# Optimization experiments

Hardware: AMD Instinct MI355X
Metric: run time of the kernel (lower is better)

The kernel has to match this reference:

```python
import jax, jax.numpy as jnp
import numpy as np

BIT = 8
QMAX = 2 ** (BIT - 1) - 1          # 127
QMIN = -(2 ** (BIT - 1))           # -128
BOUNDARY_RANGE = 0.005
EPS = 1e-5


def _quant_act_int8(x):
    # StatsQ per-tensor activation quantization: scale from (1 - boundary_range)
    # quantile of |x| (robust absmax), fake-quant with STE.
    amax = jnp.maximum(jnp.quantile(jnp.abs(x), 1.0 - BOUNDARY_RANGE), EPS)
    s = QMAX / amax
    q = jnp.clip(jnp.round(x * s), QMIN, QMAX) / s
    return x + jax.lax.stop_gradient(q - x)


def _quant_w_ternary(w):
    # BitNet-1.58-style per-tensor ternary weight quantization:
    # gamma = mean(|W|); W_q in {-1, 0, +1} * gamma; STE.
    gamma = jnp.mean(jnp.abs(w)) + EPS
    q = jnp.clip(jnp.round(w / gamma), -1.0, 1.0) * gamma
    return w + jax.lax.stop_gradient(q - w)


def _qlinear(x, w):
    # quantize activations (int8 fake-quant) and weights (ternary), then matmul
    xq = _quant_act_int8(x)
    wq = _quant_w_ternary(w)
    return jnp.einsum('btd,hd->bth', xq, wq)


def _layernorm(x, g, b):
    mu = jnp.mean(x, axis=-1, keepdims=True)
    var = jnp.mean(jnp.square(x - mu), axis=-1, keepdims=True)
    return (x - mu) * jax.lax.rsqrt(var + 1e-5) * g + b


def setup_inputs() -> dict:
    key = jax.random.key(0)
    k_x, k_w1, k_w2 = jax.random.split(key, 3)
    B, T, D, H = 64, 256, 1024, 4096
    x = jax.random.normal(k_x, (B, T, D), dtype=jnp.float32)
    ln_g = jnp.ones((D,), dtype=jnp.float32)
    ln_b = jnp.zeros((D,), dtype=jnp.float32)
    w1 = jax.random.normal(k_w1, (H, D), dtype=jnp.float32) * (1.0 / np.sqrt(D))
    w2 = jax.random.normal(k_w2, (D, H), dtype=jnp.float32) * (1.0 / np.sqrt(H))
    return {'x': x, 'ln_g': ln_g, 'ln_b': ln_b, 'w1': w1, 'w2': w2}


def reference(x, ln_g, ln_b, w1, w2):
    h = _layernorm(x, ln_g, ln_b)          # [B,T,D]
    h = _qlinear(h, w1)                    # [B,T,H]
    h = jax.nn.gelu(h, approximate=False)  # torch nn.GELU default = exact erf
    out = _qlinear(h, w2)                  # [B,T,D]
    return out
```

## Files before the change

kernel.cpp:

```cpp
#include <hip/hip_runtime.h>
#include <hip/hip_fp16.h>
#include <math.h>


#define M_ROWS 16384
#define D_DIM  1024
#define H_DIM  4096

typedef int i32x4 __attribute__((ext_vector_type(4)));
typedef int i32x16 __attribute__((ext_vector_type(16)));

#define AS1 __attribute__((address_space(1)))
#define AS3 __attribute__((address_space(3)))

__device__ __forceinline__ void load_lds16(const void* g, void* l) {
  __builtin_amdgcn_global_load_lds((const AS1 void*)g, (AS3 void*)l, 16, 0, 0);
}

__device__ __forceinline__ float block_sum256(float v, float* lds) {
#pragma unroll
  for (int o = 32; o > 0; o >>= 1) v += __shfl_down(v, o, 64);
  int t = threadIdx.x;
  __syncthreads();
  if ((t & 63) == 0) lds[t >> 6] = v;
  __syncthreads();
  return lds[0] + lds[1] + lds[2] + lds[3];
}

__global__ __launch_bounds__(256) void k_layernorm(
    const float* __restrict__ x, const float* __restrict__ g,
    const float* __restrict__ b, __half* __restrict__ out) {
  __shared__ float lds[4];
  int row = blockIdx.x, t = threadIdx.x;
  float4 v = ((const float4*)(x + (size_t)row * D_DIM))[t];
  float s = v.x + v.y + v.z + v.w;
  s = block_sum256(s, lds);
  float mu = s * (1.0f / D_DIM);
  float d0 = v.x - mu, d1 = v.y - mu, d2 = v.z - mu, d3 = v.w - mu;
  float ss = d0 * d0 + d1 * d1 + d2 * d2 + d3 * d3;
  ss = block_sum256(ss, lds);
  float inv = 1.0f / sqrtf(ss * (1.0f / D_DIM) + 1e-5f);
  float4 gg = ((const float4*)g)[t];
  float4 bb = ((const float4*)b)[t];
  __half2 p0 = __floats2half2_rn(d0 * inv * gg.x + bb.x, d1 * inv * gg.y + bb.y);
  __half2 p1 = __floats2half2_rn(d2 * inv * gg.z + bb.z, d3 * inv * gg.w + bb.w);
  uint2 st;
  st.x = *(unsigned*)&p0;
  st.y = *(unsigned*)&p1;
  ((uint2*)(out + (size_t)row * D_DIM))[t] = st;
}

__global__ __launch_bounds__(256) void k_absmean2(const float4* __restrict__ w1,
                                                  const float4* __restrict__ w2,
                                                  size_t n4, double* __restrict__ out) {
  int which = (blockIdx.x >= (gridDim.x >> 1)) ? 1 : 0;
  const float4* p = which ? w2 : w1;
  unsigned half_grid = gridDim.x >> 1;
  unsigned blk = blockIdx.x - which * half_grid;
  double s = 0.0;
  size_t stride = (size_t)half_grid * blockDim.x;
  for (size_t i = (size_t)blk * blockDim.x + threadIdx.x; i < n4; i += stride) {
    float4 v = p[i];
    s += (double)fabsf(v.x) + (double)fabsf(v.y) + (double)fabsf(v.z) + (double)fabsf(v.w);
  }
#pragma unroll
  for (int o = 32; o > 0; o >>= 1) s += __shfl_down(s, o, 64);
  __shared__ double ds[4];
  int t = threadIdx.x;
  if ((t & 63) == 0) ds[t >> 6] = s;
  __syncthreads();
  if (t == 0) atomicAdd(out + which, ds[0] + ds[1] + ds[2] + ds[3]);
}

__device__ __forceinline__ int tern1(float w, float gamma) {
  return (int)fminf(1.f, fmaxf(-1.f, rintf(w / gamma)));
}

__global__ __launch_bounds__(256) void k_wquant2(const float4* __restrict__ w1,
                                                 const float4* __restrict__ w2,
                                                 unsigned* __restrict__ q1,
                                                 unsigned* __restrict__ q2, size_t n4,
                                                 const double* __restrict__ sump,
                                                 double inv_n, float* __restrict__ gamma_out) {
  int which = (blockIdx.x >= (gridDim.x >> 1)) ? 1 : 0;
  const float4* w = which ? w2 : w1;
  unsigned* wq = which ? q2 : q1;
  unsigned half_grid = gridDim.x >> 1;
  unsigned blk = blockIdx.x - which * half_grid;
  float gamma = (float)(sump[which] * inv_n) + 1e-5f;
  if (blk == 0 && threadIdx.x == 0) gamma_out[which] = gamma;
  size_t stride = (size_t)half_grid * blockDim.x;
  for (size_t i = (size_t)blk * blockDim.x + threadIdx.x; i < n4; i += stride) {
    float4 v = w[i];
    int a = tern1(v.x, gamma), b = tern1(v.y, gamma), c = tern1(v.z, gamma), d = tern1(v.w, gamma);
    wq[i] = (unsigned)(a & 255) | ((unsigned)(b & 255) << 8) |
            ((unsigned)(c & 255) << 16) | ((unsigned)(d & 255) << 24);
  }
}

__global__ __launch_bounds__(512) void k_hist16(const uint4* __restrict__ p, size_t n8,
                                                unsigned* __restrict__ hist) {
  extern __shared__ unsigned h[];
  int t = threadIdx.x;
  for (int i = t; i < 32768; i += 512) h[i] = 0;
  __syncthreads();
  size_t stride = (size_t)gridDim.x * 512;
  for (size_t i = (size_t)blockIdx.x * 512 + t; i < n8; i += stride) {
    uint4 u = p[i];
    atomicAdd(&h[u.x & 0x7FFFu], 1u);
    atomicAdd(&h[(u.x >> 16) & 0x7FFFu], 1u);
    atomicAdd(&h[u.y & 0x7FFFu], 1u);
    atomicAdd(&h[(u.y >> 16) & 0x7FFFu], 1u);
    atomicAdd(&h[u.z & 0x7FFFu], 1u);
    atomicAdd(&h[(u.z >> 16) & 0x7FFFu], 1u);
    atomicAdd(&h[u.w & 0x7FFFu], 1u);
    atomicAdd(&h[(u.w >> 16) & 0x7FFFu], 1u);
  }
  __syncthreads();
  for (int i = t; i < 32768; i += 512) {
    unsigned c = h[i];
    if (c) atomicAdd(&hist[i], c);
  }
}

__global__ __launch_bounds__(256) void k_scanq(const unsigned* __restrict__ hist,
                                               float* __restrict__ scl,
                                               unsigned long long k, double frac) {
  __shared__ unsigned tsum[256];
  __shared__ unsigned long long pre[256];
  __shared__ unsigned vk, vk1;
  int t = threadIdx.x;
  unsigned s = 0;
  for (int j = 0; j < 128; ++j) s += hist[t * 128 + j];
  tsum[t] = s;
  __syncthreads();
  if (t == 0) {
    unsigned long long c = 0;
    for (int i = 0; i < 256; ++i) { pre[i] = c; c += tsum[i]; }
  }
  __syncthreads();
  unsigned long long base = pre[t];
  for (int j = 0; j < 128; ++j) {
    unsigned c = hist[t * 128 + j];
    if (base <= k && k < base + c) vk = t * 128 + j;
    if (base <= k + 1 && k + 1 < base + c) vk1 = t * 128 + j;
    base += c;
  }
  __syncthreads();
  if (t == 0) {
    double a = (double)__half2float(__ushort_as_half((unsigned short)vk));
    double b = (double)__half2float(__ushort_as_half((unsigned short)vk1));
    double qv = (frac >= 0.5) ? (b - (b - a) * (1.0 - frac)) : (a + (b - a) * frac);
    float amax = fmaxf((float)qv, 1e-5f);
    scl[0] = amax;
    scl[1] = 127.0f / amax;
  }
}

__device__ __forceinline__ void unpack8(uint4 u, float* f) {
  __half2 h;
  h = *(__half2*)&u.x; f[0] = __low2float(h); f[1] = __high2float(h);
  h = *(__half2*)&u.y; f[2] = __low2float(h); f[3] = __high2float(h);
  h = *(__half2*)&u.z; f[4] = __low2float(h); f[5] = __high2float(h);
  h = *(__half2*)&u.w; f[6] = __low2float(h); f[7] = __high2float(h);
}

__device__ __forceinline__ unsigned qpack4(float a, float b, float c, float d, float s) {
  int qa = (int)fminf(127.f, fmaxf(-128.f, rintf(a * s)));
  int qb = (int)fminf(127.f, fmaxf(-128.f, rintf(b * s)));
  int qc = (int)fminf(127.f, fmaxf(-128.f, rintf(c * s)));
  int qd = (int)fminf(127.f, fmaxf(-128.f, rintf(d * s)));
  return (unsigned)(qa & 255) | ((unsigned)(qb & 255) << 8) |
         ((unsigned)(qc & 255) << 16) | ((unsigned)(qd & 255) << 24);
}

__global__ __launch_bounds__(256) void k_quant16(const uint4* __restrict__ p,
                                                 uint2* __restrict__ q, size_t n8,
                                                 const float* __restrict__ scl) {
  float s = scl[1];
  size_t stride = (size_t)gridDim.x * blockDim.x;
  for (size_t i = (size_t)blockIdx.x * blockDim.x + threadIdx.x; i < n8; i += stride) {
    float f[8];
    unpack8(p[i], f);
    uint2 r;
    r.x = qpack4(f[0], f[1], f[2], f[3], s);
    r.y = qpack4(f[4], f[5], f[6], f[7], s);
    q[i] = r;
  }
}

__device__ __forceinline__ float gelu_fast(float v) {
  float a = fabsf(v) * 0.70710678118654752f;
  float t = __builtin_amdgcn_rcpf(fmaf(0.3275911f, a, 1.0f));
  float p = t * fmaf(t, fmaf(t, fmaf(t, fmaf(t, 1.061405429f, -1.453152027f),
                                     1.421413741f), -0.284496736f), 0.254829592f);
  float e = __expf(-a * a);
  float er = fmaf(-p, e, 1.0f);
  float erf_s = copysignf(er, v);
  return 0.5f * v * (1.0f + erf_s);
}

template <int K, bool GELU>
__global__ __launch_bounds__(512, 2) void k_gemm(const signed char* __restrict__ A,
                                                 const signed char* __restrict__ B,
                                                 int N, void* __restrict__ outp,
                                                 const float* __restrict__ gamma_p,
                                                 const float* __restrict__ scl) {
  constexpr int NT = K / 64;
  extern __shared__ __align__(16) char smem[];
  signed char* As = (signed char*)smem;
  signed char* Bs = (signed char*)smem + 65536;

  const int tid = threadIdx.x;
  const int lane = tid & 63;
  const int wv = tid >> 6;
  const int wr = (wv >> 2) * 128;
  const int wc = (wv & 3) * 64;

  const unsigned nwg = gridDim.x;
  const unsigned q8 = nwg >> 3;
  const unsigned bid = blockIdx.x;
  const unsigned swz = (bid & 7) * q8 + (bid >> 3);
  const unsigned nx = (unsigned)N >> 8;
  const int n0 = (int)(swz % nx) * 256;
  const int m0 = (int)(swz / nx) * 256;

  const int srow0 = tid >> 2;
  const int srow1 = srow0 + 128;
  const int scg = (tid & 3) ^ ((srow0 >> 1) & 3);
  const signed char* aG0 = A + (size_t)(m0 + srow0) * K + scg * 16;
  const signed char* aG1 = A + (size_t)(m0 + srow1) * K + scg * 16;
  const signed char* bG0 = B + (size_t)(n0 + srow0) * K + scg * 16;
  const signed char* bG1 = B + (size_t)(n0 + srow1) * K + scg * 16;
  const int sL0 = tid * 16;
  const int sL1 = sL0 + 8192;

#define STAGE_A(t_) { const int bo_ = ((t_) & 3) * 16384;            \
    load_lds16(aG0 + (size_t)(t_) * 64, As + bo_ + sL0);             \
    load_lds16(aG1 + (size_t)(t_) * 64, As + bo_ + sL1); }
#define STAGE_B(t_) { const int bo_ = ((t_) & 3) * 16384;            \
    load_lds16(bG0 + (size_t)(t_) * 64, Bs + bo_ + sL0);             \
    load_lds16(bG1 + (size_t)(t_) * 64, Bs + bo_ + sL1); }

  int a_off[4][2], b_off[2][2];
#pragma unroll
  for (int mi = 0; mi < 4; ++mi) {
    int am = wr + mi * 32 + (lane & 31);
#pragma unroll
    for (int ksl = 0; ksl < 2; ++ksl) {
      int g = ksl * 2 + (lane >> 5);
      a_off[mi][ksl] = am * 64 + ((g ^ ((am >> 1) & 3)) << 4);
    }
  }
#pragma unroll
  for (int ni = 0; ni < 2; ++ni) {
    int bn = wc + ni * 32 + (lane & 31);
#pragma unroll
    for (int ksl = 0; ksl < 2; ++ksl) {
      int g = ksl * 2 + (lane >> 5);
      b_off[ni][ksl] = bn * 64 + ((g ^ ((bn >> 1) & 3)) << 4);
    }
  }

  i32x16 acc[4][2];
#pragma unroll
  for (int mi = 0; mi < 4; ++mi)
#pragma unroll
    for (int ni = 0; ni < 2; ++ni) acc[mi][ni] = (i32x16)(0);

  STAGE_A(0); STAGE_B(0);
  STAGE_A(1); STAGE_B(1);
  STAGE_A(2); STAGE_B(2);
  asm volatile("s_waitcnt vmcnt(8)" ::: "memory");
  __builtin_amdgcn_s_barrier();

#pragma unroll 4
  for (int t = 0; t < NT; ++t) {
    const int bo = (t & 3) * 16384;
    {
      i32x4 af[4], bf[2];
#pragma unroll
      for (int mi = 0; mi < 4; ++mi) af[mi] = *(const i32x4*)(As + bo + a_off[mi][0]);
#pragma unroll
      for (int ni = 0; ni < 2; ++ni) bf[ni] = *(const i32x4*)(Bs + bo + b_off[ni][0]);
      if (t + 3 < NT) STAGE_A(t + 3);
      __builtin_amdgcn_sched_barrier(0);
      __builtin_amdgcn_s_barrier();
      __builtin_amdgcn_s_setprio(1);
#pragma unroll
      for (int mi = 0; mi < 4; ++mi)
#pragma unroll
        for (int ni = 0; ni < 2; ++ni)
          acc[mi][ni] = __builtin_amdgcn_mfma_i32_32x32x32_i8(af[mi], bf[ni], acc[mi][ni], 0, 0, 0);
      __builtin_amdgcn_s_setprio(0);
    }
    {
      i32x4 af[4], bf[2];
#pragma unroll
      for (int mi = 0; mi < 4; ++mi) af[mi] = *(const i32x4*)(As + bo + a_off[mi][1]);
#pragma unroll
      for (int ni = 0; ni < 2; ++ni) bf[ni] = *(const i32x4*)(Bs + bo + b_off[ni][1]);
      if (t + 3 < NT) STAGE_B(t + 3);
      __builtin_amdgcn_sched_barrier(0);
      __builtin_amdgcn_s_barrier();
      __builtin_amdgcn_s_setprio(1);
#pragma unroll
      for (int mi = 0; mi < 4; ++mi)
#pragma unroll
        for (int ni = 0; ni < 2; ++ni)
          acc[mi][ni] = __builtin_amdgcn_mfma_i32_32x32x32_i8(af[mi], bf[ni], acc[mi][ni], 0, 0, 0);
      __builtin_amdgcn_s_setprio(0);
    }
    if (t < NT - 3)       { asm volatile("s_waitcnt vmcnt(8)" ::: "memory"); }
    else if (t == NT - 3) { asm volatile("s_waitcnt vmcnt(4)" ::: "memory"); }
    else                  { asm volatile("s_waitcnt vmcnt(0)" ::: "memory"); }
    __builtin_amdgcn_s_barrier();
  }
#undef STAGE_A
#undef STAGE_B

  const float cs = (*gamma_p) / scl[1];
  const int col0 = n0 + wc + (lane & 31);
  const int row0 = m0 + wr + 4 * (lane >> 5);
#pragma unroll
  for (int mi = 0; mi < 4; ++mi) {
#pragma unroll
    for (int ni = 0; ni < 2; ++ni) {
      const int col = col0 + ni * 32;
#pragma unroll
      for (int reg = 0; reg < 16; ++reg) {
        const int row = row0 + mi * 32 + (reg & 3) + 8 * (reg >> 2);
        float v = cs * (float)acc[mi][ni][reg];
        size_t idx = (size_t)row * N + col;
        if (GELU) {
          ((__half*)outp)[idx] = __float2half(gelu_fast(v));
        } else {
          ((float*)outp)[idx] = v;
        }
      }
    }
  }
}

extern "C" void kernel_launch(void* const* d_in, const int* in_sizes, int n_in,
                              void* d_out, int out_size, void* d_ws, size_t ws_size,
                              hipStream_t stream) {
  const float* x = (const float*)d_in[0];
  const float* ln_g = (const float*)d_in[1];
  const float* ln_b = (const float*)d_in[2];
  const float* w1 = (const float*)d_in[3];
  const float* w2 = (const float*)d_in[4];
  float* out = (float*)d_out;

  char* ws = (char*)d_ws;
  __half* h2 = (__half*)ws;
  __half* h1 = (__half*)(ws + ((size_t)128 << 20));
  signed char* xq1 = (signed char*)(ws + ((size_t)160 << 20));
  signed char* xq2 = (signed char*)(ws + ((size_t)128 << 20));
  signed char* w1q = (signed char*)(ws + ((size_t)192 << 20));
  signed char* w2q = (signed char*)(ws + ((size_t)196 << 20));
  char* sm = ws + ((size_t)200 << 20);
  unsigned* hista = (unsigned*)sm;
  unsigned* histb = (unsigned*)(sm + (128 << 10));
  double* wsum = (double*)(sm + (256 << 10));
  float* gamma = (float*)(sm + (256 << 10) + 16);
  float* scl1 = (float*)(sm + (256 << 10) + 32);
  float* scl2 = (float*)(sm + (256 << 10) + 40);

  hipMemsetAsync(sm, 0, (256 << 10) + 64, stream);
  hipFuncSetAttribute((const void*)k_hist16, hipFuncAttributeMaxDynamicSharedMemorySize,
                      131072);
  hipFuncSetAttribute((const void*)(k_gemm<D_DIM, true>),
                      hipFuncAttributeMaxDynamicSharedMemorySize, 131072);
  hipFuncSetAttribute((const void*)(k_gemm<H_DIM, false>),
                      hipFuncAttributeMaxDynamicSharedMemorySize, 131072);

  const double qq = 1.0 - 0.005;
  const unsigned long long N1 = (unsigned long long)M_ROWS * D_DIM;
  const unsigned long long N2 = (unsigned long long)M_ROWS * H_DIM;
  double idx1 = qq * (double)(N1 - 1);
  double idx2 = qq * (double)(N2 - 1);
  unsigned long long k1 = (unsigned long long)idx1;
  unsigned long long k2 = (unsigned long long)idx2;
  double frac1 = idx1 - (double)k1;
  double frac2 = idx2 - (double)k2;

  const size_t nW4 = (size_t)H_DIM * D_DIM / 4;
  const double inv_nW = 1.0 / (double)(H_DIM * D_DIM);

  k_absmean2<<<1024, 256, 0, stream>>>((const float4*)w1, (const float4*)w2, nW4, wsum);
  k_wquant2<<<2048, 256, 0, stream>>>((const float4*)w1, (const float4*)w2,
                                      (unsigned*)w1q, (unsigned*)w2q, nW4, wsum, inv_nW, gamma);

  k_layernorm<<<M_ROWS, 256, 0, stream>>>(x, ln_g, ln_b, h1);

  const size_t n8_1 = N1 / 8;
  k_hist16<<<256, 512, 131072, stream>>>((const uint4*)h1, n8_1, hista);
  k_scanq<<<1, 256, 0, stream>>>(hista, scl1, k1, frac1);
  k_quant16<<<1024, 256, 0, stream>>>((const uint4*)h1, (uint2*)xq1, n8_1, scl1);

  k_gemm<D_DIM, true><<<(H_DIM / 256) * (M_ROWS / 256), 512, 131072, stream>>>(
      xq1, w1q, H_DIM, (void*)h2, gamma + 0, scl1);

  const size_t n8_2 = N2 / 8;
  k_hist16<<<256, 512, 131072, stream>>>((const uint4*)h2, n8_2, histb);
  k_scanq<<<1, 256, 0, stream>>>(histb, scl2, k2, frac2);
  k_quant16<<<2048, 256, 0, stream>>>((const uint4*)h2, (uint2*)xq2, n8_2, scl2);

  k_gemm<H_DIM, false><<<(D_DIM / 256) * (M_ROWS / 256), 512, 131072, stream>>>(
      xq2, w2q, D_DIM, (void*)out, gamma + 1, scl2);
}
```

Measured before the change: 494.7 us.

## Use 128-wide K tiles with double-buffered LDS and register fragment prefetch

Restructures the int8 GEMM main loop. It now stages 128-wide K slices into two LDS buffers instead of 64-wide slices into four, using an 8-way XOR swizzle. LDS reads for the next K sub-step are issued into a second set of register fragments while the MFMAs for the current sub-step run, and there is one barrier per K tile instead of two. The aim is to cut barrier and synchronization overhead and hide LDS read latency behind MFMA work. In exchange, global prefetch depth drops to a single tile, with a full vmcnt(0) wait each iteration.

```diff
diff --git a/kernel.cpp b/kernel.cpp
--- a/kernel.cpp
+++ b/kernel.cpp
@@ -206,7 +206,7 @@
                                                  int N, void* __restrict__ outp,
                                                  const float* __restrict__ gamma_p,
                                                  const float* __restrict__ scl) {
-  constexpr int NT = K / 64;
+  constexpr int NT = K / 128;
   extern __shared__ __align__(16) char smem[];
   signed char* As = (signed char*)smem;
   signed char* Bs = (signed char*)smem + 65536;
@@ -225,99 +225,107 @@
   const int n0 = (int)(swz % nx) * 256;
   const int m0 = (int)(swz / nx) * 256;
 
-  const int srow0 = tid >> 2;
-  const int srow1 = srow0 + 128;
-  const int scg = (tid & 3) ^ ((srow0 >> 1) & 3);
-  const signed char* aG0 = A + (size_t)(m0 + srow0) * K + scg * 16;
-  const signed char* aG1 = A + (size_t)(m0 + srow1) * K + scg * 16;
-  const signed char* bG0 = B + (size_t)(n0 + srow0) * K + scg * 16;
-  const signed char* bG1 = B + (size_t)(n0 + srow1) * K + scg * 16;
-  const int sL0 = tid * 16;
-  const int sL1 = sL0 + 8192;
-
-#define STAGE_A(t_) { const int bo_ = ((t_) & 3) * 16384;            \
-    load_lds16(aG0 + (size_t)(t_) * 64, As + bo_ + sL0);             \
-    load_lds16(aG1 + (size_t)(t_) * 64, As + bo_ + sL1); }
-#define STAGE_B(t_) { const int bo_ = ((t_) & 3) * 16384;            \
-    load_lds16(bG0 + (size_t)(t_) * 64, Bs + bo_ + sL0);             \
-    load_lds16(bG1 + (size_t)(t_) * 64, Bs + bo_ + sL1); }
-
-  int a_off[4][2], b_off[2][2];
+  const signed char* aG[4];
+  const signed char* bG[4];
+  int sL[4];
+#pragma unroll
+  for (int j = 0; j < 4; ++j) {
+    int g_lin = j * 512 + tid;
+    int row = g_lin >> 3;
+    int cg = (g_lin & 7) ^ (row & 7);
+    aG[j] = A + (size_t)(m0 + row) * K + cg * 16;
+    bG[j] = B + (size_t)(n0 + row) * K + cg * 16;
+    sL[j] = g_lin * 16;
+  }
+
+#define STAGE(t_)                                              \
+  {                                                            \
+    const size_t ko_ = (size_t)(t_) * 128;                     \
+    const int bo_ = ((t_) & 1) << 15;                          \
+    _Pragma("unroll") for (int j = 0; j < 4; ++j)              \
+        load_lds16(aG[j] + ko_, As + bo_ + sL[j]);             \
+    _Pragma("unroll") for (int j = 0; j < 4; ++j)              \
+        load_lds16(bG[j] + ko_, Bs + bo_ + sL[j]);             \
+  }
+
+  int a_off[4][4], b_off[2][4];
 #pragma unroll
   for (int mi = 0; mi < 4; ++mi) {
     int am = wr + mi * 32 + (lane & 31);
 #pragma unroll
-    for (int ksl = 0; ksl < 2; ++ksl) {
-      int g = ksl * 2 + (lane >> 5);
-      a_off[mi][ksl] = am * 64 + ((g ^ ((am >> 1) & 3)) << 4);
+    for (int p = 0; p < 4; ++p) {
+      int g = p * 2 + (lane >> 5);
+      a_off[mi][p] = am * 128 + ((g ^ (am & 7)) << 4);
     }
   }
 #pragma unroll
   for (int ni = 0; ni < 2; ++ni) {
     int bn = wc + ni * 32 + (lane & 31);
 #pragma unroll
-    for (int ksl = 0; ksl < 2; ++ksl) {
-      int g = ksl * 2 + (lane >> 5);
-      b_off[ni][ksl] = bn * 64 + ((g ^ ((bn >> 1) & 3)) << 4);
+    for (int p = 0; p < 4; ++p) {
+      int g = p * 2 + (lane >> 5);
+      b_off[ni][p] = bn * 128 + ((g ^ (bn & 7)) << 4);
     }
   }
 
+#define RD(fa, fb, bo_, p_)                                      \
+  {                                                              \
+    _Pragma("unroll") for (int mi = 0; mi < 4; ++mi)             \
+        fa[mi] = *(const i32x4*)(As + (bo_) + a_off[mi][p_]);    \
+    _Pragma("unroll") for (int ni = 0; ni < 2; ++ni)             \
+        fb[ni] = *(const i32x4*)(Bs + (bo_) + b_off[ni][p_]);    \
+  }
+
+#define MM(fa, fb)                                                            \
+  {                                                                           \
+    __builtin_amdgcn_s_setprio(1);                                            \
+    _Pragma("unroll") for (int mi = 0; mi < 4; ++mi)                          \
+        _Pragma("unroll") for (int ni = 0; ni < 2; ++ni)                      \
+            acc[mi][ni] = __builtin_amdgcn_mfma_i32_32x32x32_i8(              \
+                fa[mi], fb[ni], acc[mi][ni], 0, 0, 0);                        \
+    __builtin_amdgcn_s_setprio(0);                                            \
+  }
+
   i32x16 acc[4][2];
 #pragma unroll
   for (int mi = 0; mi < 4; ++mi)
 #pragma unroll
     for (int ni = 0; ni < 2; ++ni) acc[mi][ni] = (i32x16)(0);
 
-  STAGE_A(0); STAGE_B(0);
-  STAGE_A(1); STAGE_B(1);
-  STAGE_A(2); STAGE_B(2);
+  i32x4 fA0[4], fB0[2], fA1[4], fB1[2];
+
+  STAGE(0);
+  STAGE(1);
   asm volatile("s_waitcnt vmcnt(8)" ::: "memory");
   __builtin_amdgcn_s_barrier();
-
-#pragma unroll 4
+  RD(fA0, fB0, 0, 0);
+
+#pragma unroll 2
   for (int t = 0; t < NT; ++t) {
-    const int bo = (t & 3) * 16384;
-    {
-      i32x4 af[4], bf[2];
-#pragma unroll
-      for (int mi = 0; mi < 4; ++mi) af[mi] = *(const i32x4*)(As + bo + a_off[mi][0]);
-#pragma unroll
-      for (int ni = 0; ni < 2; ++ni) bf[ni] = *(const i32x4*)(Bs + bo + b_off[ni][0]);
-      if (t + 3 < NT) STAGE_A(t + 3);
-      __builtin_amdgcn_sched_barrier(0);
+    const int bo = (t & 1) << 15;
+    if (t >= 1 && t + 1 < NT) STAGE(t + 1);
+    RD(fA1, fB1, bo, 1);
+    __builtin_amdgcn_sched_barrier(0);
+    MM(fA0, fB0);
+    __builtin_amdgcn_sched_barrier(0);
+    RD(fA0, fB0, bo, 2);
+    __builtin_amdgcn_sched_barrier(0);
+    MM(fA1, fB1);
+    __builtin_amdgcn_sched_barrier(0);
+    RD(fA1, fB1, bo, 3);
+    __builtin_amdgcn_sched_barrier(0);
+    MM(fA0, fB0);
+    __builtin_amdgcn_sched_barrier(0);
+    MM(fA1, fB1);
+    if (t + 1 < NT) {
+      asm volatile("s_waitcnt vmcnt(0)" ::: "memory");
       __builtin_amdgcn_s_barrier();
-      __builtin_amdgcn_s_setprio(1);
-#pragma unroll
-      for (int mi = 0; mi < 4; ++mi)
-#pragma unroll
-        for (int ni = 0; ni < 2; ++ni)
-          acc[mi][ni] = __builtin_amdgcn_mfma_i32_32x32x32_i8(af[mi], bf[ni], acc[mi][ni], 0, 0, 0);
-      __builtin_amdgcn_s_setprio(0);
+      RD(fA0, fB0, bo ^ 32768, 0);
     }
-    {
-      i32x4 af[4], bf[2];
-#pragma unroll
-      for (int mi = 0; mi < 4; ++mi) af[mi] = *(const i32x4*)(As + bo + a_off[mi][1]);
-#pragma unroll
-      for (int ni = 0; ni < 2; ++ni) bf[ni] = *(const i32x4*)(Bs + bo + b_off[ni][1]);
-      if (t + 3 < NT) STAGE_B(t + 3);
-      __builtin_amdgcn_sched_barrier(0);
-      __builtin_amdgcn_s_barrier();
-      __builtin_amdgcn_s_setprio(1);
-#pragma unroll
-      for (int mi = 0; mi < 4; ++mi)
-#pragma unroll
-        for (int ni = 0; ni < 2; ++ni)
-          acc[mi][ni] = __builtin_amdgcn_mfma_i32_32x32x32_i8(af[mi], bf[ni], acc[mi][ni], 0, 0, 0);
-      __builtin_amdgcn_s_setprio(0);
-    }
-    if (t < NT - 3)       { asm volatile("s_waitcnt vmcnt(8)" ::: "memory"); }
-    else if (t == NT - 3) { asm volatile("s_waitcnt vmcnt(4)" ::: "memory"); }
-    else                  { asm volatile("s_waitcnt vmcnt(0)" ::: "memory"); }
-    __builtin_amdgcn_s_barrier();
-  }
-#undef STAGE_A
-#undef STAGE_B
+  }
+#undef STAGE
+#undef RD
+#undef MM
 
   const float cs = (*gamma_p) / scl[1];
   const int col0 = n0 + wc + (lane & 31);
```

New measurement: 468.2 us, median of 3. 1.06x faster.
